# Kernel optimization log

Hardware: AMD Instinct MI355X
Metric: run time of the kernel (lower is better)

The kernel has to match this reference:

```python
import jax, jax.numpy as jnp
import numpy as np

B, T, D, H = 2, 2048, 1024, 16
HD = D // H


def setup_inputs() -> dict:
    key = jax.random.key(0)
    ks = jax.random.split(key, 8)
    s = 1.0 / np.sqrt(D)
    x = jax.random.normal(ks[0], (B, T, D), dtype=jnp.float32)
    # causal additive mask, as in Whisper: -inf-like on strict upper triangle
    mask = jnp.triu(jnp.full((T, T), -1e9, dtype=jnp.float32), k=1)
    Wq = jax.random.normal(ks[1], (D, D), dtype=jnp.float32) * s
    bq = jax.random.normal(ks[2], (D,), dtype=jnp.float32) * 0.02
    Wk = jax.random.normal(ks[3], (D, D), dtype=jnp.float32) * s  # key has no bias
    Wv = jax.random.normal(ks[4], (D, D), dtype=jnp.float32) * s
    bv = jax.random.normal(ks[5], (D,), dtype=jnp.float32) * 0.02
    Wo = jax.random.normal(ks[6], (D, D), dtype=jnp.float32) * s
    bo = jax.random.normal(ks[7], (D,), dtype=jnp.float32) * 0.02
    return {"x": x, "mask": mask, "Wq": Wq, "bq": bq, "Wk": Wk,
            "Wv": Wv, "bv": bv, "Wo": Wo, "bo": bo}


def reference(x, mask, Wq, bq, Wk, Wv, bv, Wo, bo):
    # Linear layers (torch F.linear: x @ W.T + b)
    q = x @ Wq.T + bq                      # [B, T, D]
    k = x @ Wk.T                           # [B, T, D] (no bias)
    v = x @ Wv.T + bv                      # [B, T, D]

    scale = (D // H) ** (-0.25)
    qh = q.reshape(B, T, H, HD) * scale    # [B, T, H, hd]
    kh = k.reshape(B, T, H, HD) * scale
    vh = v.reshape(B, T, H, HD)

    qk = jnp.einsum("bqhd,bkhd->bhqk", qh, kh)        # [B, H, T, T]
    qk = qk + mask[:T, :T]
    w = jax.nn.softmax(qk.astype(jnp.float32), axis=-1).astype(q.dtype)
    wv = jnp.einsum("bhqk,bkhd->bqhd", w, vh).reshape(B, T, D)
    return wv @ Wo.T + bo
```

## Files before the change

kernel.cpp:

```cpp
#include <hip/hip_runtime.h>
#include <hip/hip_bf16.h>

#define B_ 2
#define T_ 2048
#define D_ 1024
#define H_ 16
#define HD_ 64

typedef __attribute__((ext_vector_type(8))) short bf16x8;
typedef __attribute__((ext_vector_type(4))) short bf16x4;
typedef __attribute__((ext_vector_type(4))) float f32x4;
typedef __attribute__((ext_vector_type(4))) unsigned int u32x4;

__device__ __forceinline__ short f2bf(float f) {
  unsigned int u = __builtin_bit_cast(unsigned int, f);
  u += 0x7fffu + ((u >> 16) & 1u);
  return (short)(u >> 16);
}

__device__ __forceinline__ unsigned cvtpk(float lo, float hi) {
  unsigned r;
  asm("v_cvt_pk_bf16_f32 %0, %1, %2" : "=v"(r) : "v"(lo), "v"(hi));
  return r;
}

__device__ __forceinline__ float ex2(float x) {
  float r;
  asm("v_exp_f32 %0, %1" : "=v"(r) : "v"(x));
  return r;
}

__device__ __forceinline__ void gl16(const short* g, short* l) {
  __builtin_amdgcn_global_load_lds(
      (const __attribute__((address_space(1))) void*)g,
      (__attribute__((address_space(3))) void*)l, 16, 0, 0);
}

__global__ void cast_all(const float* __restrict__ x,
                         const float* __restrict__ w0, const float* __restrict__ w1,
                         const float* __restrict__ w2, const float* __restrict__ w3,
                         short* __restrict__ out) {
  int i = (blockIdx.x * blockDim.x + threadIdx.x) * 8;
  const float* src;
  int off;
  if (i < 4194304) { src = x; off = i; }
  else {
    int j = i - 4194304;
    int seg = j >> 20;
    src = (seg == 0) ? w0 : (seg == 1) ? w1 : (seg == 2) ? w2 : w3;
    off = j & 1048575;
  }
  float4 a = *(const float4*)(src + off);
  float4 b = *(const float4*)(src + off + 4);
  bf16x8 o;
  o[0] = f2bf(a.x); o[1] = f2bf(a.y); o[2] = f2bf(a.z); o[3] = f2bf(a.w);
  o[4] = f2bf(b.x); o[5] = f2bf(b.y); o[6] = f2bf(b.z); o[7] = f2bf(b.w);
  *(bf16x8*)(out + i) = o;
}

__launch_bounds__(256, 3)
__global__ void gemm_qkv(const short* __restrict__ A, const short* __restrict__ W,
                         const float* __restrict__ bq, const float* __restrict__ bv,
                         short* __restrict__ Qb, short* __restrict__ Kb,
                         short* __restrict__ Vtb) {
  __shared__ short As[2][64 * 64];
  __shared__ short Bs[2][128 * 64];
  const int xcd = blockIdx.x & 7, g = blockIdx.x >> 3;
  const int bm = (xcd >> 1) * 16 + (g & 15);
  const int bn = (xcd & 1) * 12 + (g >> 4);
  const int tid = threadIdx.x, lane = tid & 63, w = tid >> 6;
  const int wr = w >> 1, wc = w & 1;
  const int lrow = lane & 15, lhi = lane >> 4;
  const int srow = lane >> 3, sch = lane & 7;
  const int swz = (lrow & 7) << 3;

  f32x4 acc[2][4] = {};
  auto STAGE = [&](int kt, int buf) {
#pragma unroll
    for (int i = 0; i < 2; ++i) {
      int row = w * 16 + i * 8 + srow;
      gl16(A + (size_t)(bm * 64 + row) * 1024 + kt + ((sch ^ (row & 7)) * 8),
           &As[buf][(w * 16 + i * 8) * 64]);
    }
#pragma unroll
    for (int i = 0; i < 4; ++i) {
      int row = w * 32 + i * 8 + srow;
      gl16(W + (size_t)(bn * 128 + row) * 1024 + kt + ((sch ^ (row & 7)) * 8),
           &Bs[buf][(w * 32 + i * 8) * 64]);
    }
  };

  STAGE(0, 0);
  for (int t = 0; t < 16; ++t) {
    const int buf = t & 1;
    if (t < 15) {
      STAGE((t + 1) * 64, buf ^ 1);
      asm volatile("s_waitcnt vmcnt(6)" ::: "memory");
    } else {
      asm volatile("s_waitcnt vmcnt(0)" ::: "memory");
    }
    __builtin_amdgcn_s_barrier();
    bf16x8 af[2][2], bfr[2][4];
#pragma unroll
    for (int ks = 0; ks < 2; ++ks) {
#pragma unroll
      for (int i = 0; i < 2; ++i)
        af[ks][i] = *(const bf16x8*)(&As[buf][(wr * 32 + i * 16 + lrow) * 64 + ((ks * 32 + lhi * 8) ^ swz)]);
#pragma unroll
      for (int j = 0; j < 4; ++j)
        bfr[ks][j] = *(const bf16x8*)(&Bs[buf][(wc * 64 + j * 16 + lrow) * 64 + ((ks * 32 + lhi * 8) ^ swz)]);
    }
#pragma unroll
    for (int ks = 0; ks < 2; ++ks)
#pragma unroll
      for (int i = 0; i < 2; ++i)
#pragma unroll
        for (int j = 0; j < 4; ++j)
          acc[i][j] = __builtin_amdgcn_mfma_f32_16x16x32_bf16(af[ks][i], bfr[ks][j],
                                                              acc[i][j], 0, 0, 0);
    asm volatile("s_waitcnt lgkmcnt(0)" ::: "memory");
    __builtin_amdgcn_s_barrier();
  }

#pragma unroll
  for (int i = 0; i < 2; ++i)
#pragma unroll
    for (int j = 0; j < 4; ++j) {
      const int m0 = bm * 64 + wr * 32 + i * 16 + lhi * 4;
      const int n = bn * 128 + wc * 64 + j * 16 + lrow;
      const int seg = n >> 10, nloc = n & 1023;
      const int h = nloc >> 6, hd = nloc & 63;
      const int b = m0 >> 11, t0 = m0 & 2047;
      if (seg == 0) {
        float bb = bq[nloc];
#pragma unroll
        for (int r = 0; r < 4; ++r)
          Qb[((size_t)(b * H_ + h) * T_ + t0 + r) * HD_ + hd] =
              f2bf((acc[i][j][r] + bb) * 0.180336880f);
      } else if (seg == 1) {
#pragma unroll
        for (int r = 0; r < 4; ++r)
          Kb[((size_t)(b * H_ + h) * T_ + t0 + r) * HD_ + hd] = f2bf(acc[i][j][r]);
      } else {
        float bb = bv[nloc];
        bf16x4 ov;
#pragma unroll
        for (int r = 0; r < 4; ++r) ov[r] = f2bf(acc[i][j][r] + bb);
        const int c = wr * 32 + lhi * 8 + i * 4;
        *(bf16x4*)(Vtb + ((size_t)(b * H_ + h) * HD_ + hd) * T_ + (t0 & ~63) + c) = ov;
      }
    }
}

__launch_bounds__(256, 3)
__global__ void gemm_o(const short* __restrict__ A, const short* __restrict__ W,
                       const float* __restrict__ bias, float* __restrict__ out) {
  __shared__ short As[2][64 * 64];
  __shared__ short Bs[2][128 * 64];
  const int xcd = blockIdx.x & 7, g = blockIdx.x >> 3;
  const int bm = (xcd >> 1) * 16 + (g & 15);
  const int bn = (xcd & 1) * 4 + (g >> 4);
  const int tid = threadIdx.x, lane = tid & 63, w = tid >> 6;
  const int wr = w >> 1, wc = w & 1;
  const int lrow = lane & 15, lhi = lane >> 4;
  const int srow = lane >> 3, sch = lane & 7;
  const int swz = (lrow & 7) << 3;

  f32x4 acc[2][4] = {};
  auto STAGE = [&](int kt, int buf) {
#pragma unroll
    for (int i = 0; i < 2; ++i) {
      int row = w * 16 + i * 8 + srow;
      gl16(A + (size_t)(bm * 64 + row) * 1024 + kt + ((sch ^ (row & 7)) * 8),
           &As[buf][(w * 16 + i * 8) * 64]);
    }
#pragma unroll
    for (int i = 0; i < 4; ++i) {
      int row = w * 32 + i * 8 + srow;
      gl16(W + (size_t)(bn * 128 + row) * 1024 + kt + ((sch ^ (row & 7)) * 8),
           &Bs[buf][(w * 32 + i * 8) * 64]);
    }
  };

  STAGE(0, 0);
  for (int t = 0; t < 16; ++t) {
    const int buf = t & 1;
    if (t < 15) {
      STAGE((t + 1) * 64, buf ^ 1);
      asm volatile("s_waitcnt vmcnt(6)" ::: "memory");
    } else {
      asm volatile("s_waitcnt vmcnt(0)" ::: "memory");
    }
    __builtin_amdgcn_s_barrier();
    bf16x8 af[2][2], bfr[2][4];
#pragma unroll
    for (int ks = 0; ks < 2; ++ks) {
#pragma unroll
      for (int i = 0; i < 2; ++i)
        af[ks][i] = *(const bf16x8*)(&As[buf][(wr * 32 + i * 16 + lrow) * 64 + ((ks * 32 + lhi * 8) ^ swz)]);
#pragma unroll
      for (int j = 0; j < 4; ++j)
        bfr[ks][j] = *(const bf16x8*)(&Bs[buf][(wc * 64 + j * 16 + lrow) * 64 + ((ks * 32 + lhi * 8) ^ swz)]);
    }
#pragma unroll
    for (int ks = 0; ks < 2; ++ks)
#pragma unroll
      for (int i = 0; i < 2; ++i)
#pragma unroll
        for (int j = 0; j < 4; ++j)
          acc[i][j] = __builtin_amdgcn_mfma_f32_16x16x32_bf16(af[ks][i], bfr[ks][j],
                                                              acc[i][j], 0, 0, 0);
    asm volatile("s_waitcnt lgkmcnt(0)" ::: "memory");
    __builtin_amdgcn_s_barrier();
  }

#pragma unroll
  for (int i = 0; i < 2; ++i)
#pragma unroll
    for (int j = 0; j < 4; ++j) {
      const int m0 = bm * 64 + wr * 32 + i * 16 + lhi * 4;
      const int n = bn * 128 + wc * 64 + j * 16 + lrow;
      const float bb = bias[n];
#pragma unroll
      for (int r = 0; r < 4; ++r)
        out[(size_t)(m0 + r) * 1024 + n] = acc[i][j][r] + bb;
    }
}

__launch_bounds__(256, 4)
__global__ void attn_kernel(const short* __restrict__ Q, const short* __restrict__ K,
                            const short* __restrict__ Vt, short* __restrict__ Ob) {
  __shared__ short Ks_[2][64 * 64];
  __shared__ short Vs_[2][64 * 64];
  const int tid = threadIdx.x, lane = tid & 63, w = tid >> 6;
  const int lrow = lane & 15, lhi = lane >> 4;
  const int bid = blockIdx.x;
  const int bh = (bid & 7) * 4 + ((bid >> 3) & 3);
  const int x = bid >> 5, g = x & 7, q = x >> 3;
  const int tile = ((q & 1) ? (7 - g) : g) * 4 + q;
  const int b = bh >> 4, h = bh & 15;
  const short* Kbh = K + (size_t)bh * T_ * HD_;
  const short* Vbh = Vt + (size_t)bh * HD_ * T_;

  bf16x8 qf[2];
#pragma unroll
  for (int ks = 0; ks < 2; ++ks)
    qf[ks] = *(const bf16x8*)(Q + ((size_t)bh * T_ + tile * 64 + w * 16 + lrow) * HD_ + ks * 32 + lhi * 8);

  f32x4 oacc[4] = {};
  float lrun = 0.f;
  const int qlocal = w * 16 + lrow;
  const int srow8 = lane >> 3, sch = lane & 7;
  const int swz = (lrow & 7) << 3;

  auto STAGE = [&](int kb, int buf) {
#pragma unroll
    for (int pass = 0; pass < 2; ++pass) {
      int row = pass * 32 + w * 8 + srow8;
      int csrc = (sch ^ (row & 7)) * 8;
      gl16(Kbh + (size_t)(kb * 64 + row) * HD_ + csrc, &Ks_[buf][(pass * 32 + w * 8) * 64]);
      gl16(Vbh + (size_t)row * T_ + kb * 64 + csrc, &Vs_[buf][(pass * 32 + w * 8) * 64]);
    }
  };

  STAGE(0, 0);
  int cur = 0;
  for (int kb = 0; kb <= tile; ++kb) {
    asm volatile("s_waitcnt vmcnt(0) lgkmcnt(0)" ::: "memory");
    __builtin_amdgcn_s_barrier();
    asm volatile("" ::: "memory");
    const short* Kc = Ks_[cur];
    const short* Vc = Vs_[cur];
    bf16x8 kf[4][2];
#pragma unroll
    for (int n = 0; n < 4; ++n)
#pragma unroll
      for (int ks = 0; ks < 2; ++ks)
        kf[n][ks] = *(const bf16x8*)(Kc + (n * 16 + lrow) * 64 + ((ks * 32 + lhi * 8) ^ swz));
    bf16x8 vf[4][2];
#pragma unroll
    for (int j = 0; j < 4; ++j)
#pragma unroll
      for (int ks = 0; ks < 2; ++ks)
        vf[j][ks] = *(const bf16x8*)(Vc + (j * 16 + lrow) * 64 + ((ks * 32 + lhi * 8) ^ swz));
    if (kb < tile) STAGE(kb + 1, cur ^ 1);

    f32x4 s[4] = {};
    __builtin_amdgcn_s_setprio(1);
#pragma unroll
    for (int n = 0; n < 4; ++n)
#pragma unroll
      for (int ks = 0; ks < 2; ++ks)
        s[n] = __builtin_amdgcn_mfma_f32_16x16x32_bf16(kf[n][ks], qf[ks], s[n], 0, 0, 0);
    __builtin_amdgcn_s_setprio(0);

    if (kb == tile) {
#pragma unroll
      for (int n = 0; n < 4; ++n)
#pragma unroll
        for (int r = 0; r < 4; ++r)
          if (n * 16 + lhi * 4 + r > qlocal) s[n][r] = -1e9f;
    }

    float p[4][4];
    float ls = 0.f;
#pragma unroll
    for (int n = 0; n < 4; ++n)
#pragma unroll
      for (int r = 0; r < 4; ++r) {
        float e = ex2(s[n][r]);
        p[n][r] = e;
        ls += e;
      }
    lrun += ls;

    u32x4 pw0, pw1;
    pw0[0] = cvtpk(p[0][0], p[0][1]); pw0[1] = cvtpk(p[0][2], p[0][3]);
    pw0[2] = cvtpk(p[1][0], p[1][1]); pw0[3] = cvtpk(p[1][2], p[1][3]);
    pw1[0] = cvtpk(p[2][0], p[2][1]); pw1[1] = cvtpk(p[2][2], p[2][3]);
    pw1[2] = cvtpk(p[3][0], p[3][1]); pw1[3] = cvtpk(p[3][2], p[3][3]);
    bf16x8 pf0 = __builtin_bit_cast(bf16x8, pw0);
    bf16x8 pf1 = __builtin_bit_cast(bf16x8, pw1);

    __builtin_amdgcn_s_setprio(1);
#pragma unroll
    for (int j = 0; j < 4; ++j) {
      oacc[j] = __builtin_amdgcn_mfma_f32_16x16x32_bf16(vf[j][0], pf0, oacc[j], 0, 0, 0);
      oacc[j] = __builtin_amdgcn_mfma_f32_16x16x32_bf16(vf[j][1], pf1, oacc[j], 0, 0, 0);
    }
    __builtin_amdgcn_s_setprio(0);
    cur ^= 1;
  }

  lrun += __shfl_xor(lrun, 16);
  lrun += __shfl_xor(lrun, 32);
  float inv = 1.0f / lrun;
  const int t = tile * 64 + qlocal;
#pragma unroll
  for (int j = 0; j < 4; ++j) {
    bf16x4 ok;
#pragma unroll
    for (int r = 0; r < 4; ++r) ok[r] = f2bf(oacc[j][r] * inv);
    *(bf16x4*)(Ob + (size_t)(b * T_ + t) * D_ + h * 64 + j * 16 + lhi * 4) = ok;
  }
}

extern "C" void kernel_launch(void* const* d_in, const int* in_sizes, int n_in,
                              void* d_out, int out_size, void* d_ws, size_t ws_size,
                              hipStream_t stream) {
  const float* x  = (const float*)d_in[0];
  const float* Wq = (const float*)d_in[2];
  const float* bq = (const float*)d_in[3];
  const float* Wk = (const float*)d_in[4];
  const float* Wv = (const float*)d_in[5];
  const float* bv = (const float*)d_in[6];
  const float* Wo = (const float*)d_in[7];
  const float* bo = (const float*)d_in[8];
  float* out = (float*)d_out;

  const int MT = B_ * T_;
  short* xb  = (short*)d_ws;
  short* wqb = xb  + (size_t)MT * D_;
  short* wob = wqb + (size_t)3 * D_ * D_;
  short* Qb  = wob + (size_t)D_ * D_;
  short* Kb  = Qb  + (size_t)MT * D_;
  short* Vtb = Kb  + (size_t)MT * D_;
  short* Ab  = Vtb + (size_t)MT * D_;

  cast_all<<<(8 * 1048576) / (256 * 8), 256, 0, stream>>>(x, Wq, Wk, Wv, Wo, xb);

  gemm_qkv<<<(MT / 64) * 24, 256, 0, stream>>>(xb, wqb, bq, bv, Qb, Kb, Vtb);

  attn_kernel<<<B_ * H_ * 32, 256, 0, stream>>>(Qb, Kb, Vtb, Ab);

  gemm_o<<<(MT / 64) * 8, 256, 0, stream>>>(Ab, wob, bo, out);
}
```

Measured before the change: 90.74 us.

## Process two query tiles per attention block to reuse staged K/V

Each attention block now handles 128 query rows as two 64-row halves that share every staged K/V tile from LDS. This halves the global-to-LDS traffic and barrier count per query row. The tile-to-block mapping changes to pair short and long causal ranges, and the grid is halved. The cost is more registers per thread (two sets of accumulators and Q fragments) and fewer blocks in flight, which can lower occupancy and parallelism.

```diff
diff --git a/kernel.cpp b/kernel.cpp
--- a/kernel.cpp
+++ b/kernel.cpp
@@ -237,18 +237,20 @@
   const int bid = blockIdx.x;
   const int bh = (bid & 7) * 4 + ((bid >> 3) & 3);
   const int x = bid >> 5, g = x & 7, q = x >> 3;
-  const int tile = ((q & 1) ? (7 - g) : g) * 4 + q;
+  const int tile = q ? (15 - g) : g;
   const int b = bh >> 4, h = bh & 15;
   const short* Kbh = K + (size_t)bh * T_ * HD_;
   const short* Vbh = Vt + (size_t)bh * HD_ * T_;
 
-  bf16x8 qf[2];
-#pragma unroll
-  for (int ks = 0; ks < 2; ++ks)
-    qf[ks] = *(const bf16x8*)(Q + ((size_t)bh * T_ + tile * 64 + w * 16 + lrow) * HD_ + ks * 32 + lhi * 8);
-
-  f32x4 oacc[4] = {};
-  float lrun = 0.f;
+  bf16x8 qfA[2], qfB[2];
+#pragma unroll
+  for (int ks = 0; ks < 2; ++ks) {
+    qfA[ks] = *(const bf16x8*)(Q + ((size_t)bh * T_ + tile * 128 + w * 16 + lrow) * HD_ + ks * 32 + lhi * 8);
+    qfB[ks] = *(const bf16x8*)(Q + ((size_t)bh * T_ + tile * 128 + 64 + w * 16 + lrow) * HD_ + ks * 32 + lhi * 8);
+  }
+
+  f32x4 oaccA[4] = {}, oaccB[4] = {};
+  float lrunA = 0.f, lrunB = 0.f;
   const int qlocal = w * 16 + lrow;
   const int srow8 = lane >> 3, sch = lane & 7;
   const int swz = (lrow & 7) << 3;
@@ -263,85 +265,130 @@
     }
   };
 
+  const int kb_last = 2 * tile + 1;
   STAGE(0, 0);
   int cur = 0;
-  for (int kb = 0; kb <= tile; ++kb) {
+  for (int kb = 0; kb <= kb_last; ++kb) {
     asm volatile("s_waitcnt vmcnt(0) lgkmcnt(0)" ::: "memory");
     __builtin_amdgcn_s_barrier();
     asm volatile("" ::: "memory");
     const short* Kc = Ks_[cur];
     const short* Vc = Vs_[cur];
-    bf16x8 kf[4][2];
+    bf16x8 kf[4][2], vf[4][2];
 #pragma unroll
     for (int n = 0; n < 4; ++n)
 #pragma unroll
+      for (int ks = 0; ks < 2; ++ks) {
+        kf[n][ks] = *(const bf16x8*)(Kc + (n * 16 + lrow) * 64 + ((ks * 32 + lhi * 8) ^ swz));
+        vf[n][ks] = *(const bf16x8*)(Vc + (n * 16 + lrow) * 64 + ((ks * 32 + lhi * 8) ^ swz));
+      }
+    if (kb < kb_last) STAGE(kb + 1, cur ^ 1);
+
+    const bool actA = (kb <= kb_last - 1);
+    f32x4 sB[4] = {}, sA[4] = {};
+    __builtin_amdgcn_s_setprio(1);
+#pragma unroll
+    for (int n = 0; n < 4; ++n)
+#pragma unroll
       for (int ks = 0; ks < 2; ++ks)
-        kf[n][ks] = *(const bf16x8*)(Kc + (n * 16 + lrow) * 64 + ((ks * 32 + lhi * 8) ^ swz));
-    bf16x8 vf[4][2];
-#pragma unroll
-    for (int j = 0; j < 4; ++j)
-#pragma unroll
-      for (int ks = 0; ks < 2; ++ks)
-        vf[j][ks] = *(const bf16x8*)(Vc + (j * 16 + lrow) * 64 + ((ks * 32 + lhi * 8) ^ swz));
-    if (kb < tile) STAGE(kb + 1, cur ^ 1);
-
-    f32x4 s[4] = {};
-    __builtin_amdgcn_s_setprio(1);
-#pragma unroll
-    for (int n = 0; n < 4; ++n)
-#pragma unroll
-      for (int ks = 0; ks < 2; ++ks)
-        s[n] = __builtin_amdgcn_mfma_f32_16x16x32_bf16(kf[n][ks], qf[ks], s[n], 0, 0, 0);
+        sB[n] = __builtin_amdgcn_mfma_f32_16x16x32_bf16(kf[n][ks], qfB[ks], sB[n], 0, 0, 0);
+    if (actA) {
+#pragma unroll
+      for (int n = 0; n < 4; ++n)
+#pragma unroll
+        for (int ks = 0; ks < 2; ++ks)
+          sA[n] = __builtin_amdgcn_mfma_f32_16x16x32_bf16(kf[n][ks], qfA[ks], sA[n], 0, 0, 0);
+    }
     __builtin_amdgcn_s_setprio(0);
 
-    if (kb == tile) {
+    if (kb == kb_last) {
 #pragma unroll
       for (int n = 0; n < 4; ++n)
 #pragma unroll
         for (int r = 0; r < 4; ++r)
-          if (n * 16 + lhi * 4 + r > qlocal) s[n][r] = -1e9f;
-    }
-
-    float p[4][4];
-    float ls = 0.f;
-#pragma unroll
-    for (int n = 0; n < 4; ++n)
-#pragma unroll
-      for (int r = 0; r < 4; ++r) {
-        float e = ex2(s[n][r]);
-        p[n][r] = e;
-        ls += e;
+          if (n * 16 + lhi * 4 + r > qlocal) sB[n][r] = -1e9f;
+    }
+    if (actA && kb == kb_last - 1) {
+#pragma unroll
+      for (int n = 0; n < 4; ++n)
+#pragma unroll
+        for (int r = 0; r < 4; ++r)
+          if (n * 16 + lhi * 4 + r > qlocal) sA[n][r] = -1e9f;
+    }
+
+    {
+      float p[4][4];
+      float ls = 0.f;
+#pragma unroll
+      for (int n = 0; n < 4; ++n)
+#pragma unroll
+        for (int r = 0; r < 4; ++r) {
+          float e = ex2(sB[n][r]);
+          p[n][r] = e;
+          ls += e;
+        }
+      lrunB += ls;
+      u32x4 pw0, pw1;
+      pw0[0] = cvtpk(p[0][0], p[0][1]); pw0[1] = cvtpk(p[0][2], p[0][3]);
+      pw0[2] = cvtpk(p[1][0], p[1][1]); pw0[3] = cvtpk(p[1][2], p[1][3]);
+      pw1[0] = cvtpk(p[2][0], p[2][1]); pw1[1] = cvtpk(p[2][2], p[2][3]);
+      pw1[2] = cvtpk(p[3][0], p[3][1]); pw1[3] = cvtpk(p[3][2], p[3][3]);
+      bf16x8 pf0 = __builtin_bit_cast(bf16x8, pw0);
+      bf16x8 pf1 = __builtin_bit_cast(bf16x8, pw1);
+      __builtin_amdgcn_s_setprio(1);
+#pragma unroll
+      for (int j = 0; j < 4; ++j) {
+        oaccB[j] = __builtin_amdgcn_mfma_f32_16x16x32_bf16(vf[j][0], pf0, oaccB[j], 0, 0, 0);
+        oaccB[j] = __builtin_amdgcn_mfma_f32_16x16x32_bf16(vf[j][1], pf1, oaccB[j], 0, 0, 0);
       }
-    lrun += ls;
-
-    u32x4 pw0, pw1;
-    pw0[0] = cvtpk(p[0][0], p[0][1]); pw0[1] = cvtpk(p[0][2], p[0][3]);
-    pw0[2] = cvtpk(p[1][0], p[1][1]); pw0[3] = cvtpk(p[1][2], p[1][3]);
-    pw1[0] = cvtpk(p[2][0], p[2][1]); pw1[1] = cvtpk(p[2][2], p[2][3]);
-    pw1[2] = cvtpk(p[3][0], p[3][1]); pw1[3] = cvtpk(p[3][2], p[3][3]);
-    bf16x8 pf0 = __builtin_bit_cast(bf16x8, pw0);
-    bf16x8 pf1 = __builtin_bit_cast(bf16x8, pw1);
-
-    __builtin_amdgcn_s_setprio(1);
-#pragma unroll
-    for (int j = 0; j < 4; ++j) {
-      oacc[j] = __builtin_amdgcn_mfma_f32_16x16x32_bf16(vf[j][0], pf0, oacc[j], 0, 0, 0);
-      oacc[j] = __builtin_amdgcn_mfma_f32_16x16x32_bf16(vf[j][1], pf1, oacc[j], 0, 0, 0);
-    }
-    __builtin_amdgcn_s_setprio(0);
+      __builtin_amdgcn_s_setprio(0);
+    }
+    if (actA) {
+      float p[4][4];
+      float ls = 0.f;
+#pragma unroll
+      for (int n = 0; n < 4; ++n)
+#pragma unroll
+        for (int r = 0; r < 4; ++r) {
+          float e = ex2(sA[n][r]);
+          p[n][r] = e;
+          ls += e;
+        }
+      lrunA += ls;
+      u32x4 pw0, pw1;
+      pw0[0] = cvtpk(p[0][0], p[0][1]); pw0[1] = cvtpk(p[0][2], p[0][3]);
+      pw0[2] = cvtpk(p[1][0], p[1][1]); pw0[3] = cvtpk(p[1][2], p[1][3]);
+      pw1[0] = cvtpk(p[2][0], p[2][1]); pw1[1] = cvtpk(p[2][2], p[2][3]);
+      pw1[2] = cvtpk(p[3][0], p[3][1]); pw1[3] = cvtpk(p[3][2], p[3][3]);
+      bf16x8 pf0 = __builtin_bit_cast(bf16x8, pw0);
+      bf16x8 pf1 = __builtin_bit_cast(bf16x8, pw1);
+      __builtin_amdgcn_s_setprio(1);
+#pragma unroll
+      for (int j = 0; j < 4; ++j) {
+        oaccA[j] = __builtin_amdgcn_mfma_f32_16x16x32_bf16(vf[j][0], pf0, oaccA[j], 0, 0, 0);
+        oaccA[j] = __builtin_amdgcn_mfma_f32_16x16x32_bf16(vf[j][1], pf1, oaccA[j], 0, 0, 0);
+      }
+      __builtin_amdgcn_s_setprio(0);
+    }
     cur ^= 1;
   }
 
-  lrun += __shfl_xor(lrun, 16);
-  lrun += __shfl_xor(lrun, 32);
-  float inv = 1.0f / lrun;
-  const int t = tile * 64 + qlocal;
+  lrunA += __shfl_xor(lrunA, 16);
+  lrunA += __shfl_xor(lrunA, 32);
+  lrunB += __shfl_xor(lrunB, 16);
+  lrunB += __shfl_xor(lrunB, 32);
+  float invA = 1.0f / lrunA, invB = 1.0f / lrunB;
+  const int tA = tile * 128 + qlocal, tB = tile * 128 + 64 + qlocal;
 #pragma unroll
   for (int j = 0; j < 4; ++j) {
-    bf16x4 ok;
-#pragma unroll
-    for (int r = 0; r < 4; ++r) ok[r] = f2bf(oacc[j][r] * inv);
-    *(bf16x4*)(Ob + (size_t)(b * T_ + t) * D_ + h * 64 + j * 16 + lhi * 4) = ok;
+    bf16x4 oA, oB;
+#pragma unroll
+    for (int r = 0; r < 4; ++r) {
+      oA[r] = f2bf(oaccA[j][r] * invA);
+      oB[r] = f2bf(oaccB[j][r] * invB);
+    }
+    *(bf16x4*)(Ob + (size_t)(b * T_ + tA) * D_ + h * 64 + j * 16 + lhi * 4) = oA;
+    *(bf16x4*)(Ob + (size_t)(b * T_ + tB) * D_ + h * 64 + j * 16 + lhi * 4) = oB;
   }
 }
 
@@ -371,7 +418,7 @@
 
   gemm_qkv<<<(MT / 64) * 24, 256, 0, stream>>>(xb, wqb, bq, bv, Qb, Kb, Vtb);
 
-  attn_kernel<<<B_ * H_ * 32, 256, 0, stream>>>(Qb, Kb, Vtb, Ab);
+  attn_kernel<<<B_ * H_ * 16, 256, 0, stream>>>(Qb, Kb, Vtb, Ab);
 
   gemm_o<<<(MT / 64) * 8, 256, 0, stream>>>(Ab, wob, bo, out);
 }
```

Measured after the change: 145.5 us. 1.6x slower.
